# Kernel tuning notes

Measured on AMD Instinct MI355X. Metric: run time of the kernel, lower is better.

## Reference

```python
import jax, jax.numpy as jnp
import numpy as np

IN_F = 128
OUT_F = 128
N_NODES = 50000
N_EDGES = 800000


def setup_inputs() -> dict:
    key = jax.random.key(0)
    k_x, k_e, k_w, k_b = jax.random.split(key, 4)
    x = jax.random.normal(k_x, (N_NODES, IN_F), dtype=jnp.float32)
    edge_index = jax.random.randint(k_e, (2, N_EDGES), 0, N_NODES, dtype=jnp.int64)
    # linear params (torch nn.Linear: y = x @ W.T + b)
    bound = 1.0 / np.sqrt(IN_F)
    W = jax.random.uniform(k_w, (OUT_F, IN_F), minval=-bound, maxval=bound, dtype=jnp.float32)
    b = jax.random.uniform(k_b, (OUT_F,), minval=-bound, maxval=bound, dtype=jnp.float32)
    return {"x": x, "edge_index": edge_index, "n_nodes": N_NODES, "W": W, "b": b}


def reference(x, edge_index, n_nodes, W, b):
    row, col = edge_index[0], edge_index[1]
    # gather source features and segment-sum into destination nodes
    agg = jax.ops.segment_sum(x[row], col, num_segments=n_nodes)  # [N, in_f]
    # in-degree, clamped to 1 (bincount + clamp in torch)
    deg = jax.ops.segment_sum(jnp.ones_like(col, dtype=jnp.float32), col, num_segments=n_nodes)
    deg = jnp.maximum(deg, 1.0)
    h = agg / deg[:, None]
    return h @ W.T + b
```

## Files before the change

### kernel.cpp

```cpp
#include <hip/hip_runtime.h>

#define IN_F 128
#define OUT_F 128

typedef unsigned int uint32;
typedef unsigned short ushort16;
using short8 = __attribute__((ext_vector_type(8))) short;
using f32x4  = __attribute__((ext_vector_type(4))) float;
using vint4  = __attribute__((ext_vector_type(4))) int;

__device__ __forceinline__ uint32 f2bf(float f) {
    const uint32 u = __float_as_uint(f);
    return (u + 0x7FFFu + ((u >> 16) & 1u)) >> 16;
}
__device__ __forceinline__ uint32 pack_bf2(float lo, float hi) {
    return f2bf(lo) | (f2bf(hi) << 16);
}
__device__ __forceinline__ float bflo(uint32 u) { return __uint_as_float(u << 16); }
__device__ __forceinline__ float bfhi(uint32 u) { return __uint_as_float(u & 0xFFFF0000u); }

__global__ __launch_bounds__(256) void k_prep(
    const float* __restrict__ x, const float* __restrict__ W,
    uint32* __restrict__ xb, uint32* __restrict__ wb,
    int* __restrict__ deg_i, int nx4, int nw4, int nNodes)
{
    const int i4 = blockIdx.x * 256 + threadIdx.x;
    if (i4 < nNodes) deg_i[i4] = 0;
    if (i4 < nx4) {
        const float4 v = reinterpret_cast<const float4*>(x)[i4];
        uint2 st;
        st.x = pack_bf2(v.x, v.y);
        st.y = pack_bf2(v.z, v.w);
        reinterpret_cast<uint2*>(xb)[i4] = st;
    } else if (i4 - nx4 < nw4) {
        const int j4 = i4 - nx4;
        const float4 v = reinterpret_cast<const float4*>(W)[j4];
        uint2 st;
        st.x = pack_bf2(v.x, v.y);
        st.y = pack_bf2(v.z, v.w);
        reinterpret_cast<uint2*>(wb)[j4] = st;
    }
}

__global__ __launch_bounds__(256) void k_hist(
    const int* __restrict__ ei, int* __restrict__ deg_i, int nEdges)
{
    int e = blockIdx.x * blockDim.x + threadIdx.x;
    if (e < nEdges) {
        const int dst = __builtin_nontemporal_load(ei + nEdges + e);
        atomicAdd(&deg_i[dst], 1);
    }
}

__global__ __launch_bounds__(256) void k_scan_a(
    const int* __restrict__ deg_i, int* __restrict__ escan,
    int* __restrict__ bsum, int n)
{
    __shared__ int sh[256];
    const int t = threadIdx.x;
    const int i = blockIdx.x * 256 + t;
    int v = (i < n) ? deg_i[i] : 0;
    sh[t] = v;
    __syncthreads();
    for (int ofs = 1; ofs < 256; ofs <<= 1) {
        int u = (t >= ofs) ? sh[t - ofs] : 0;
        __syncthreads();
        sh[t] += u;
        __syncthreads();
    }
    if (i < n) escan[i] = sh[t] - v;
    if (t == 255) bsum[blockIdx.x] = sh[255];
}

__global__ __launch_bounds__(256) void k_scan_c(
    const int* __restrict__ escan, const int* __restrict__ bsum,
    int* __restrict__ off, int* __restrict__ cursor, int n, int nsb)
{
    __shared__ int sh[256];
    const int t = threadIdx.x;
    const int b = blockIdx.x;

    sh[t] = (t < nsb) ? bsum[t] : 0;
    __syncthreads();
    for (int ofs = 1; ofs < 256; ofs <<= 1) {
        int u = (t >= ofs) ? sh[t - ofs] : 0;
        __syncthreads();
        sh[t] += u;
        __syncthreads();
    }
    const int prefix = (b == 0) ? 0 : sh[b - 1];

    const int i = b * 256 + t;
    if (i < n) {
        const int o = escan[i] + prefix;
        off[i] = o;
        cursor[i] = o;
    }
}

__global__ __launch_bounds__(256) void k_scatter_ids(
    const int* __restrict__ ei, int* __restrict__ cursor,
    unsigned short* __restrict__ perm, int nEdges)
{
    const int cls = blockIdx.x & 7;
    const int e0 = ((blockIdx.x >> 3) * 256 + threadIdx.x) * 4;
    if (e0 >= nEdges) return;

    if (e0 + 4 <= nEdges) {
        const vint4 dst4 = __builtin_nontemporal_load(
            reinterpret_cast<const vint4*>(ei + nEdges + e0));
        if (((dst4.x >> 7) & 7) == cls) {
            const int p = atomicAdd(&cursor[dst4.x], 1);
            perm[p] = (unsigned short)ei[e0 + 0];
        }
        if (((dst4.y >> 7) & 7) == cls) {
            const int p = atomicAdd(&cursor[dst4.y], 1);
            perm[p] = (unsigned short)ei[e0 + 1];
        }
        if (((dst4.z >> 7) & 7) == cls) {
            const int p = atomicAdd(&cursor[dst4.z], 1);
            perm[p] = (unsigned short)ei[e0 + 2];
        }
        if (((dst4.w >> 7) & 7) == cls) {
            const int p = atomicAdd(&cursor[dst4.w], 1);
            perm[p] = (unsigned short)ei[e0 + 3];
        }
    } else {
        for (int e = e0; e < nEdges; ++e) {
            const int dst = ei[nEdges + e];
            if (((dst >> 7) & 7) == cls) {
                const int p = atomicAdd(&cursor[dst], 1);
                perm[p] = (unsigned short)ei[e];
            }
        }
    }
}

__global__ __launch_bounds__(256) void k_gather(
    const uint32* __restrict__ xb2,
    const unsigned short* __restrict__ perm,
    const int* __restrict__ off,
    const int* __restrict__ deg_i,
    uint32* __restrict__ hb2,
    int nNodes)
{
    const int wv   = blockIdx.x * 4 + (threadIdx.x >> 6);
    const int lane = threadIdx.x & 63;
    const int n0 = wv * 2;
    if (n0 >= nNodes) return;
    const int n1 = n0 + 1;
    const bool has1 = (n1 < nNodes);

    const int s0 = off[n0];
    const int d0 = deg_i[n0];
    const int s1 = has1 ? off[n1] : 0;
    const int d1 = has1 ? deg_i[n1] : 0;

    float ax0 = 0.f, ay0 = 0.f, ax1 = 0.f, ay1 = 0.f;
    int i0 = 0, i1 = 0;

    for (; i0 + 2 <= d0 && i1 + 2 <= d1; i0 += 2, i1 += 2) {
        const int p00 = perm[s0 + i0];
        const int p01 = perm[s0 + i0 + 1];
        const int p10 = perm[s1 + i1];
        const int p11 = perm[s1 + i1 + 1];
        const uint32 a = xb2[(size_t)p00 * 64 + lane];
        const uint32 b = xb2[(size_t)p01 * 64 + lane];
        const uint32 c = xb2[(size_t)p10 * 64 + lane];
        const uint32 d = xb2[(size_t)p11 * 64 + lane];
        ax0 += bflo(a) + bflo(b);
        ay0 += bfhi(a) + bfhi(b);
        ax1 += bflo(c) + bflo(d);
        ay1 += bfhi(c) + bfhi(d);
    }
    for (; i0 + 4 <= d0; i0 += 4) {
        const uint32 a = xb2[(size_t)perm[s0 + i0 + 0] * 64 + lane];
        const uint32 b = xb2[(size_t)perm[s0 + i0 + 1] * 64 + lane];
        const uint32 c = xb2[(size_t)perm[s0 + i0 + 2] * 64 + lane];
        const uint32 d = xb2[(size_t)perm[s0 + i0 + 3] * 64 + lane];
        ax0 += bflo(a) + bflo(b) + bflo(c) + bflo(d);
        ay0 += bfhi(a) + bfhi(b) + bfhi(c) + bfhi(d);
    }
    for (; i0 < d0; ++i0) {
        const uint32 a = xb2[(size_t)perm[s0 + i0] * 64 + lane];
        ax0 += bflo(a);
        ay0 += bfhi(a);
    }
    for (; i1 + 4 <= d1; i1 += 4) {
        const uint32 a = xb2[(size_t)perm[s1 + i1 + 0] * 64 + lane];
        const uint32 b = xb2[(size_t)perm[s1 + i1 + 1] * 64 + lane];
        const uint32 c = xb2[(size_t)perm[s1 + i1 + 2] * 64 + lane];
        const uint32 d = xb2[(size_t)perm[s1 + i1 + 3] * 64 + lane];
        ax1 += bflo(a) + bflo(b) + bflo(c) + bflo(d);
        ay1 += bfhi(a) + bfhi(b) + bfhi(c) + bfhi(d);
    }
    for (; i1 < d1; ++i1) {
        const uint32 a = xb2[(size_t)perm[s1 + i1] * 64 + lane];
        ax1 += bflo(a);
        ay1 += bfhi(a);
    }

    const float inv0 = 1.0f / (float)(d0 > 0 ? d0 : 1);
    hb2[(size_t)n0 * 64 + lane] = pack_bf2(ax0 * inv0, ay0 * inv0);
    if (has1) {
        const float inv1 = 1.0f / (float)(d1 > 0 ? d1 : 1);
        hb2[(size_t)n1 * 64 + lane] = pack_bf2(ax1 * inv1, ay1 * inv1);
    }
}

__global__ __launch_bounds__(256) void k_mm(
    const ushort16* __restrict__ hbf,
    const ushort16* __restrict__ wbf,
    const float* __restrict__ bias,
    float* __restrict__ out, int nNodes)
{
    const int wave = threadIdx.x >> 6;
    const int lane = threadIdx.x & 63;
    const int m0 = blockIdx.x * 128 + wave * 32;
    const int lrow = lane & 15;
    const int kgrp = lane >> 4;

    short8 a[2][4];
#pragma unroll
    for (int mt = 0; mt < 2; ++mt) {
        int mrow = m0 + mt * 16 + lrow;
        if (mrow >= nNodes) mrow = nNodes - 1;
        const ushort16* hrow = hbf + (size_t)mrow * IN_F;
#pragma unroll
        for (int kt = 0; kt < 4; ++kt) {
            a[mt][kt] = *reinterpret_cast<const short8*>(hrow + kt * 32 + kgrp * 8);
        }
    }

#pragma unroll
    for (int nt = 0; nt < 8; ++nt) {
        const int n0 = nt * 16;
        const ushort16* wrow = wbf + (size_t)(n0 + lrow) * IN_F;
        const float bv = bias[n0 + lrow];

        f32x4 acc0 = {bv, bv, bv, bv};
        f32x4 acc1 = {bv, bv, bv, bv};
#pragma unroll
        for (int kt = 0; kt < 4; ++kt) {
            const short8 b = *reinterpret_cast<const short8*>(wrow + kt * 32 + kgrp * 8);
            acc0 = __builtin_amdgcn_mfma_f32_16x16x32_bf16(a[0][kt], b, acc0, 0, 0, 0);
            acc1 = __builtin_amdgcn_mfma_f32_16x16x32_bf16(a[1][kt], b, acc1, 0, 0, 0);
        }
#pragma unroll
        for (int r = 0; r < 4; ++r) {
            const int row0 = m0 + kgrp * 4 + r;
            const int row1 = m0 + 16 + kgrp * 4 + r;
            if (row0 < nNodes) out[(size_t)row0 * OUT_F + n0 + lrow] = acc0[r];
            if (row1 < nNodes) out[(size_t)row1 * OUT_F + n0 + lrow] = acc1[r];
        }
    }
}

extern "C" void kernel_launch(void* const* d_in, const int* in_sizes, int n_in,
                              void* d_out, int out_size, void* d_ws, size_t ws_size,
                              hipStream_t stream)
{
    const float* x   = (const float*)d_in[0];
    const int*   ei  = (const int*)d_in[1];
    const float* W   = (const float*)d_in[3];
    const float* b   = (const float*)d_in[4];
    float*       out = (float*)d_out;

    const int nNodes = in_sizes[0] / IN_F;
    const int nEdges = in_sizes[1] / 2;
    const int nsb = (nNodes + 255) / 256;

    int* deg_i  = (int*)d_ws;
    int* off    = deg_i + nNodes;
    int* cursor = off + nNodes;
    int* escan  = cursor + nNodes;
    int* bsum   = escan + nNodes;
    unsigned short* perm = (unsigned short*)(bsum + nsb);
    ushort16* hbf = (ushort16*)(perm + nEdges);
    ushort16* wbf = hbf + (size_t)nNodes * IN_F;

    uint32* xb = (uint32*)d_out;

    const int nx4 = (nNodes * IN_F) / 4;
    const int nw4 = (OUT_F * IN_F) / 4;
    k_prep<<<(nx4 + nw4 + 255) / 256, 256, 0, stream>>>(
        x, W, xb, (uint32*)wbf, deg_i, nx4, nw4, nNodes);

    const int eb = (nEdges + 255) / 256;
    k_hist<<<eb, 256, 0, stream>>>(ei, deg_i, nEdges);

    k_scan_a<<<nsb, 256, 0, stream>>>(deg_i, escan, bsum, nNodes);
    k_scan_c<<<nsb, 256, 0, stream>>>(escan, bsum, off, cursor, nNodes, nsb);

    const int chunks = (nEdges + 1023) / 1024;
    k_scatter_ids<<<chunks * 8, 256, 0, stream>>>(ei, cursor, perm, nEdges);

    const int nPairs = (nNodes + 1) / 2;
    const int gb = (nPairs + 3) / 4;
    k_gather<<<gb, 256, 0, stream>>>(xb, perm, off, deg_i, (uint32*)hbf, nNodes);

    const int mb = (nNodes + 127) / 128;
    k_mm<<<mb, 256, 0, stream>>>(hbf, wbf, b, out, nNodes);
}
```

Baseline: 144.4 us.

## Pre-bin edges by destination class during histogram, then scatter from compact bins

New measurement: 142.2 us. Within noise of the previous version (-1.5%).

```diff
diff --git a/kernel.cpp b/kernel.cpp
--- a/kernel.cpp
+++ b/kernel.cpp
@@ -2,6 +2,8 @@
 
 #define IN_F 128
 #define OUT_F 128
+#define BIN_EPB 2048
+#define CAP 131072
 
 typedef unsigned int uint32;
 typedef unsigned short ushort16;
@@ -22,10 +24,12 @@
 __global__ __launch_bounds__(256) void k_prep(
     const float* __restrict__ x, const float* __restrict__ W,
     uint32* __restrict__ xb, uint32* __restrict__ wb,
-    int* __restrict__ deg_i, int nx4, int nw4, int nNodes)
+    int* __restrict__ deg_i, int* __restrict__ gcur,
+    int nx4, int nw4, int nNodes)
 {
     const int i4 = blockIdx.x * 256 + threadIdx.x;
     if (i4 < nNodes) deg_i[i4] = 0;
+    if (i4 < 8) gcur[i4] = 0;
     if (i4 < nx4) {
         const float4 v = reinterpret_cast<const float4*>(x)[i4];
         uint2 st;
@@ -42,13 +46,58 @@
     }
 }
 
-__global__ __launch_bounds__(256) void k_hist(
-    const int* __restrict__ ei, int* __restrict__ deg_i, int nEdges)
-{
-    int e = blockIdx.x * blockDim.x + threadIdx.x;
-    if (e < nEdges) {
-        const int dst = __builtin_nontemporal_load(ei + nEdges + e);
-        atomicAdd(&deg_i[dst], 1);
+__global__ __launch_bounds__(256) void k_bin8(
+    const int* __restrict__ ei, int* __restrict__ deg_i,
+    int* __restrict__ gcur, uint32* __restrict__ gseg, int nEdges)
+{
+    __shared__ int lcount[8], lbase[8], lplace[8];
+    const int t = threadIdx.x;
+    if (t < 8) { lcount[t] = 0; lplace[t] = 0; }
+    __syncthreads();
+
+    const int base = blockIdx.x * BIN_EPB;
+    uint32 ent[8];
+    int ecls[8];
+
+#pragma unroll
+    for (int k = 0; k < 2; ++k) {
+        const int e0 = base + (k * 256 + t) * 4;
+        if (e0 + 4 <= nEdges) {
+            const vint4 s4 = *reinterpret_cast<const vint4*>(ei + e0);
+            const vint4 d4 = *reinterpret_cast<const vint4*>(ei + nEdges + e0);
+            ent[k * 4 + 0] = ((uint32)d4.x << 16) | (uint32)s4.x;
+            ent[k * 4 + 1] = ((uint32)d4.y << 16) | (uint32)s4.y;
+            ent[k * 4 + 2] = ((uint32)d4.z << 16) | (uint32)s4.z;
+            ent[k * 4 + 3] = ((uint32)d4.w << 16) | (uint32)s4.w;
+            ecls[k * 4 + 0] = (d4.x >> 7) & 7;
+            ecls[k * 4 + 1] = (d4.y >> 7) & 7;
+            ecls[k * 4 + 2] = (d4.z >> 7) & 7;
+            ecls[k * 4 + 3] = (d4.w >> 7) & 7;
+        } else {
+#pragma unroll
+            for (int j = 0; j < 4; ++j) ecls[k * 4 + j] = -1;
+        }
+    }
+
+#pragma unroll
+    for (int k = 0; k < 8; ++k) {
+        if (ecls[k] >= 0) {
+            atomicAdd(&lcount[ecls[k]], 1);
+            atomicAdd(&deg_i[ent[k] >> 16], 1);
+        }
+    }
+    __syncthreads();
+
+    if (t < 8) lbase[t] = atomicAdd(&gcur[t], lcount[t]);
+    __syncthreads();
+
+#pragma unroll
+    for (int k = 0; k < 8; ++k) {
+        if (ecls[k] >= 0) {
+            const int c = ecls[k];
+            const int r = atomicAdd(&lplace[c], 1);
+            gseg[(size_t)c * CAP + lbase[c] + r] = ent[k];
+        }
     }
 }
 
@@ -98,39 +147,34 @@
     }
 }
 
-__global__ __launch_bounds__(256) void k_scatter_ids(
-    const int* __restrict__ ei, int* __restrict__ cursor,
-    unsigned short* __restrict__ perm, int nEdges)
+__global__ __launch_bounds__(256) void k_scatter2(
+    const uint32* __restrict__ gseg, const int* __restrict__ gcur,
+    int* __restrict__ cursor, unsigned short* __restrict__ perm)
 {
     const int cls = blockIdx.x & 7;
-    const int e0 = ((blockIdx.x >> 3) * 256 + threadIdx.x) * 4;
-    if (e0 >= nEdges) return;
-
-    if (e0 + 4 <= nEdges) {
-        const vint4 dst4 = __builtin_nontemporal_load(
-            reinterpret_cast<const vint4*>(ei + nEdges + e0));
-        if (((dst4.x >> 7) & 7) == cls) {
-            const int p = atomicAdd(&cursor[dst4.x], 1);
-            perm[p] = (unsigned short)ei[e0 + 0];
-        }
-        if (((dst4.y >> 7) & 7) == cls) {
-            const int p = atomicAdd(&cursor[dst4.y], 1);
-            perm[p] = (unsigned short)ei[e0 + 1];
-        }
-        if (((dst4.z >> 7) & 7) == cls) {
-            const int p = atomicAdd(&cursor[dst4.z], 1);
-            perm[p] = (unsigned short)ei[e0 + 2];
-        }
-        if (((dst4.w >> 7) & 7) == cls) {
-            const int p = atomicAdd(&cursor[dst4.w], 1);
-            perm[p] = (unsigned short)ei[e0 + 3];
-        }
-    } else {
-        for (int e = e0; e < nEdges; ++e) {
-            const int dst = ei[nEdges + e];
-            if (((dst >> 7) & 7) == cls) {
+    const int slice = blockIdx.x >> 3;
+    const int cnt = gcur[cls];
+    const uint32* __restrict__ seg = gseg + (size_t)cls * CAP;
+
+    const int stride = 64 * 256 * 4;
+    for (int j0 = (slice * 256 + threadIdx.x) * 4; j0 < cnt; j0 += stride) {
+        if (j0 + 4 <= cnt) {
+            const vint4 e4 = *reinterpret_cast<const vint4*>(seg + j0);
+#pragma unroll
+            for (int j = 0; j < 4; ++j) {
+                const uint32 e = (j == 0) ? (uint32)e4.x :
+                                 (j == 1) ? (uint32)e4.y :
+                                 (j == 2) ? (uint32)e4.z : (uint32)e4.w;
+                const int dst = (int)(e >> 16);
                 const int p = atomicAdd(&cursor[dst], 1);
-                perm[p] = (unsigned short)ei[e];
+                perm[p] = (unsigned short)(e & 0xFFFFu);
+            }
+        } else {
+            for (int j = j0; j < cnt; ++j) {
+                const uint32 e = seg[j];
+                const int dst = (int)(e >> 16);
+                const int p = atomicAdd(&cursor[dst], 1);
+                perm[p] = (unsigned short)(e & 0xFFFFu);
             }
         }
     }
@@ -270,12 +314,14 @@
     const int nEdges = in_sizes[1] / 2;
     const int nsb = (nNodes + 255) / 256;
 
-    int* deg_i  = (int*)d_ws;
-    int* off    = deg_i + nNodes;
-    int* cursor = off + nNodes;
-    int* escan  = cursor + nNodes;
-    int* bsum   = escan + nNodes;
-    unsigned short* perm = (unsigned short*)(bsum + nsb);
+    int*    deg_i = (int*)d_ws;
+    int*    off   = deg_i + nNodes;
+    int*    cursor= off + nNodes;
+    int*    escan = cursor + nNodes;
+    int*    bsum  = escan + nNodes;
+    int*    gcur  = bsum + nsb;
+    uint32* gseg  = (uint32*)(gcur + 8);
+    unsigned short* perm = (unsigned short*)(gseg + (size_t)8 * CAP);
     ushort16* hbf = (ushort16*)(perm + nEdges);
     ushort16* wbf = hbf + (size_t)nNodes * IN_F;
 
@@ -284,16 +330,15 @@
     const int nx4 = (nNodes * IN_F) / 4;
     const int nw4 = (OUT_F * IN_F) / 4;
     k_prep<<<(nx4 + nw4 + 255) / 256, 256, 0, stream>>>(
-        x, W, xb, (uint32*)wbf, deg_i, nx4, nw4, nNodes);
-
-    const int eb = (nEdges + 255) / 256;
-    k_hist<<<eb, 256, 0, stream>>>(ei, deg_i, nEdges);
+        x, W, xb, (uint32*)wbf, deg_i, gcur, nx4, nw4, nNodes);
+
+    const int binb = (nEdges + BIN_EPB - 1) / BIN_EPB;
+    k_bin8<<<binb, 256, 0, stream>>>(ei, deg_i, gcur, gseg, nEdges);
 
     k_scan_a<<<nsb, 256, 0, stream>>>(deg_i, escan, bsum, nNodes);
     k_scan_c<<<nsb, 256, 0, stream>>>(escan, bsum, off, cursor, nNodes, nsb);
 
-    const int chunks = (nEdges + 1023) / 1024;
-    k_scatter_ids<<<chunks * 8, 256, 0, stream>>>(ei, cursor, perm, nEdges);
+    k_scatter2<<<512, 256, 0, stream>>>(gseg, gcur, cursor, perm);
 
     const int nPairs = (nNodes + 1) / 2;
     const int gb = (nPairs + 3) / 4;
```
